# Kernel optimization log

Hardware: AMD Instinct MI355X
Metric: run time of the kernel (lower is better)

The kernel has to match this reference:

```python
import jax, jax.numpy as jnp
import numpy as np

N_QUBITS = 6
N_LAYERS = 3
FEATURE_DIM = 512
ENC_HIDDEN = max(32, N_QUBITS * 4)  # 32
HEAD_HIDDEN = 128
G, T = 54, 24
DIM = 2 ** N_QUBITS  # 64


def _ry_batched(angles):
    # angles: [B] -> batched RY matrices [B, 2, 2] (complex64)
    c = jnp.cos(angles * 0.5)
    s = jnp.sin(angles * 0.5)
    U = jnp.stack([jnp.stack([c, -s], -1), jnp.stack([s, c], -1)], -2)
    return U.astype(jnp.complex64)


def _rot(phi, theta, omega):
    # PennyLane Rot = RZ(omega) RY(theta) RZ(phi); returns [2, 2] complex64
    c = jnp.cos(theta * 0.5).astype(jnp.complex64)
    s = jnp.sin(theta * 0.5).astype(jnp.complex64)
    ep = jnp.exp(-0.5j * (phi + omega).astype(jnp.complex64))  # e^{-i(phi+omega)/2}
    em = jnp.exp(-0.5j * (phi - omega).astype(jnp.complex64))  # e^{-i(phi-omega)/2}
    u00 = ep * c
    u01 = -jnp.conj(em) * s
    u10 = em * s
    u11 = jnp.conj(ep) * c
    return jnp.stack([jnp.stack([u00, u01]), jnp.stack([u10, u11])])


def _apply_1q_batched(state, U, q):
    # state: [B, 2^n]; U: [B, 2, 2] (per-sample gate, e.g. data-encoding RY)
    B = state.shape[0]
    st = state.reshape(B, 2 ** q, 2, -1)
    st = jnp.einsum('bij,bljr->blir', U, st)
    return st.reshape(B, -1)


def _apply_1q(state, U, q):
    # state: [B, 2^n]; U: [2, 2] shared across batch (trainable Rot)
    B = state.shape[0]
    st = state.reshape(B, 2 ** q, 2, -1)
    st = jnp.einsum('ij,bljr->blir', U, st)
    return st.reshape(B, -1)


def _apply_cnot(state, c, t):
    # state: [B, 2^n]; flip target axis where control bit == 1
    B = state.shape[0]
    st = state.reshape((B,) + (2,) * N_QUBITS)
    ax_c, ax_t = 1 + c, 1 + t
    s0 = jnp.take(st, 0, axis=ax_c)
    s1 = jnp.take(st, 1, axis=ax_c)
    s1 = jnp.flip(s1, axis=ax_t if ax_t < ax_c else ax_t - 1)
    st = jnp.stack([s0, s1], axis=ax_c)
    return st.reshape(B, -1)


def _expvals_z(state):
    # <Z_q> for every qubit: [B, n]
    B = state.shape[0]
    probs = (state.real ** 2 + state.imag ** 2).reshape((B,) + (2,) * N_QUBITS)
    outs = []
    for q in range(N_QUBITS):
        axes = tuple(i for i in range(1, N_QUBITS + 1) if i != q + 1)
        p = probs.sum(axes)  # [B, 2]
        outs.append(p[:, 0] - p[:, 1])
    return jnp.stack(outs, -1)


def _circuit(angles, q_weights):
    # angles: [B, n_qubits] float32; q_weights: [L, n, 3]
    B = angles.shape[0]
    state = jnp.zeros((B, DIM), jnp.complex64).at[:, 0].set(1.0)
    for layer in range(N_LAYERS):
        # data_reuploading=True -> re-encode every layer
        for q in range(N_QUBITS):
            state = _apply_1q_batched(state, _ry_batched(angles[:, q]), q)
        for q in range(N_QUBITS):
            w = q_weights[layer, q]
            state = _apply_1q(state, _rot(w[0], w[1], w[2]), q)
        for q in range(0, N_QUBITS - 1, 2):
            state = _apply_cnot(state, q, q + 1)
        for q in range(1, N_QUBITS - 1, 2):
            state = _apply_cnot(state, q, q + 1)
        state = _apply_cnot(state, N_QUBITS - 1, 0)  # n_qubits > 2
    return _expvals_z(state)


def setup_inputs() -> dict:
    key = jax.random.key(0)
    ks = jax.random.split(key, 10)
    B = 32768
    return {
        'x': jax.random.normal(ks[0], (B, FEATURE_DIM), jnp.float32),
        'enc_w1': 0.05 * jax.random.normal(ks[1], (FEATURE_DIM, ENC_HIDDEN), jnp.float32),
        'enc_b1': jnp.zeros((ENC_HIDDEN,), jnp.float32),
        'enc_w2': 0.05 * jax.random.normal(ks[2], (ENC_HIDDEN, N_QUBITS), jnp.float32),
        'enc_b2': jnp.zeros((N_QUBITS,), jnp.float32),
        'q_weights': 0.01 * jax.random.normal(ks[3], (N_LAYERS, N_QUBITS, 3), jnp.float32),
        'head_w1': 0.1 * jax.random.normal(ks[4], (N_QUBITS, HEAD_HIDDEN), jnp.float32),
        'head_b1': jnp.zeros((HEAD_HIDDEN,), jnp.float32),
        'head_w2': 0.05 * jax.random.normal(ks[5], (HEAD_HIDDEN, G * T), jnp.float32),
        'head_b2': jnp.zeros((G * T,), jnp.float32),
    }


def reference(x, enc_w1, enc_b1, enc_w2, enc_b2, q_weights,
              head_w1, head_b1, head_w2, head_b2):
    # classical encoder -> angles [B, n_qubits]
    h = jnp.tanh(x @ enc_w1 + enc_b1)
    angles = h @ enc_w2 + enc_b2
    # batched state-vector PQC simulation
    z = _circuit(angles, q_weights).astype(jnp.float32)  # [B, n_qubits]
    # classical head (dropout is identity in eval)
    g = jax.nn.relu(z @ head_w1 + head_b1)
    logits = g @ head_w2 + head_b2
    return logits.reshape(-1, G, T)
```

## Files before the change

kernel.cpp:

```cpp
#include <hip/hip_runtime.h>

typedef __bf16 bf16x8 __attribute__((ext_vector_type(8)));
typedef float floatx4 __attribute__((ext_vector_type(4)));
typedef unsigned short ushort8 __attribute__((ext_vector_type(8)));

__device__ __forceinline__ unsigned short f2bf(float f) {
    unsigned u = __float_as_uint(f);
    u += 0x7fffu + ((u >> 16) & 1u);
    return (unsigned short)(u >> 16);
}

template <int ST>
__device__ __forceinline__ void apply_g(float* sr, float* si,
    float m00r, float m00i, float m01r, float m01i,
    float m10r, float m10i, float m11r, float m11i) {
#pragma unroll
    for (int i = 0; i < 64; ++i) {
        if ((i & ST) == 0) {
            int i1 = i + ST;
            float r0 = sr[i], u0 = si[i], r1 = sr[i1], u1 = si[i1];
            sr[i]  = m00r * r0 - m00i * u0 + m01r * r1 - m01i * u1;
            si[i]  = m00r * u0 + m00i * r0 + m01r * u1 + m01i * r1;
            sr[i1] = m10r * r0 - m10i * u0 + m11r * r1 - m11i * u1;
            si[i1] = m10r * u0 + m10i * r0 + m11r * u1 + m11i * r1;
        }
    }
}

template <int CB, int TB>
__device__ __forceinline__ void cnot_g(float* sr, float* si) {
#pragma unroll
    for (int i = 0; i < 64; ++i) {
        if ((i & CB) && !(i & TB)) {
            int i1 = i + TB;
            float tr = sr[i]; sr[i] = sr[i1]; sr[i1] = tr;
            float ti = si[i]; si[i] = si[i1]; si[i1] = ti;
        }
    }
}

__global__ __launch_bounds__(256) void fused_front(
    const float* __restrict__ x, const float* __restrict__ w1,
    const float* __restrict__ b1, const float* __restrict__ w2,
    const float* __restrict__ b2, const float* __restrict__ qw,
    const float* __restrict__ hw1, const float* __restrict__ hb1,
    const float* __restrict__ hw2,
    unsigned short* __restrict__ w2t, unsigned short* __restrict__ g) {

    if (blockIdx.x >= 512) {
        int t = (blockIdx.x - 512) * 256 + threadIdx.x;
        int nn = t >> 4;
        int kc = (t & 15) * 8;
        if (nn < 1296) {
            ushort8 pk;
#pragma unroll
            for (int j = 0; j < 8; ++j) pk[j] = f2bf(hw2[(size_t)(kc + j) * 1296 + nn]);
            *(ushort8*)(w2t + (size_t)nn * 128 + kc) = pk;
        }
        return;
    }

    __shared__ float part[4][64][33];
    __shared__ float hsh[64][33];
    __shared__ float umat_s[144];

    if (threadIdx.x < 18) {
        int t = threadIdx.x;
        float phi = qw[t * 3], theta = qw[t * 3 + 1], omega = qw[t * 3 + 2];
        float c = cosf(0.5f * theta), s = sinf(0.5f * theta);
        float po = 0.5f * (phi + omega), pm = 0.5f * (phi - omega);
        float epr = cosf(po), epi = -sinf(po);
        float emr = cosf(pm), emi = -sinf(pm);
        float* u = umat_s + t * 8;
        u[0] = epr * c;  u[1] = epi * c;
        u[2] = -emr * s; u[3] = emi * s;
        u[4] = emr * s;  u[5] = emi * s;
        u[6] = epr * c;  u[7] = -epi * c;
    }

    int lane = threadIdx.x & 63;
    int wave = threadIdx.x >> 6;
    int swave = __builtin_amdgcn_readfirstlane(wave);
    size_t row = (size_t)blockIdx.x * 64 + lane;
    const float2* x2 = (const float2*)(x + row * 512 + swave * 128);
    const float* wseg = w1 + swave * 128 * 32;

    float acc[32];
#pragma unroll
    for (int j = 0; j < 32; ++j) acc[j] = 0.f;

#pragma clang loop unroll(disable)
    for (int k2 = 0; k2 < 64; ++k2) {
        float2 xv = x2[k2];
        const float* wr = wseg + k2 * 64;
#pragma unroll
        for (int j = 0; j < 32; ++j) acc[j] = fmaf(wr[j], xv.x, acc[j]);
#pragma unroll
        for (int j = 0; j < 32; ++j) acc[j] = fmaf(wr[32 + j], xv.y, acc[j]);
    }
#pragma unroll
    for (int j = 0; j < 32; ++j) part[wave][lane][j] = acc[j];
    __syncthreads();

    int rl = threadIdx.x & 63;
    int jg = (threadIdx.x >> 6) * 8;
#pragma unroll
    for (int jj = 0; jj < 8; ++jj) {
        int j = jg + jj;
        float v = part[0][rl][j] + part[1][rl][j] + part[2][rl][j] + part[3][rl][j] + b1[j];
        hsh[rl][j] = tanhf(v);
    }
    __syncthreads();

    if (threadIdx.x >= 64) return;

    float h[32];
#pragma unroll
    for (int j = 0; j < 32; ++j) h[j] = hsh[threadIdx.x][j];
    float ca[6], sa[6];
#pragma unroll
    for (int q = 0; q < 6; ++q) {
        float a = b2[q];
#pragma unroll
        for (int j = 0; j < 32; ++j) a = fmaf(h[j], w2[j * 6 + q], a);
        a = 0.5f * a;
        ca[q] = cosf(a);
        sa[q] = sinf(a);
    }

    float sr[64], si[64];
#pragma unroll
    for (int i = 0; i < 64; ++i) { sr[i] = 0.f; si[i] = 0.f; }
    sr[0] = 1.f;

#pragma clang loop unroll(disable)
    for (int layer = 0; layer < 3; ++layer) {
        const float* ub = umat_s + layer * 48;
#define DOQ(Q, ST) {                                                      \
        const float* u = ub + (Q) * 8;                                    \
        float c = ca[Q], ss = sa[Q];                                      \
        float m00r = u[0] * c + u[2] * ss, m00i = u[1] * c + u[3] * ss;   \
        float m01r = u[2] * c - u[0] * ss, m01i = u[3] * c - u[1] * ss;   \
        float m10r = u[4] * c + u[6] * ss, m10i = u[5] * c + u[7] * ss;   \
        float m11r = u[6] * c - u[4] * ss, m11i = u[7] * c - u[5] * ss;   \
        apply_g<ST>(sr, si, m00r, m00i, m01r, m01i, m10r, m10i, m11r, m11i); }
        DOQ(0, 32) DOQ(1, 16) DOQ(2, 8) DOQ(3, 4) DOQ(4, 2) DOQ(5, 1)
#undef DOQ
        cnot_g<32, 16>(sr, si);
        cnot_g<8, 4>(sr, si);
        cnot_g<2, 1>(sr, si);
        cnot_g<16, 8>(sr, si);
        cnot_g<4, 2>(sr, si);
        cnot_g<1, 32>(sr, si);
    }

    float z[6] = {0.f, 0.f, 0.f, 0.f, 0.f, 0.f};
#pragma unroll
    for (int i = 0; i < 64; ++i) {
        float p = sr[i] * sr[i] + si[i] * si[i];
        z[0] += (i & 32) ? -p : p;
        z[1] += (i & 16) ? -p : p;
        z[2] += (i & 8)  ? -p : p;
        z[3] += (i & 4)  ? -p : p;
        z[4] += (i & 2)  ? -p : p;
        z[5] += (i & 1)  ? -p : p;
    }

    int s = blockIdx.x * 64 + threadIdx.x;
    unsigned short* gp = g + (size_t)s * 128;
#pragma unroll 2
    for (int j0 = 0; j0 < 128; j0 += 8) {
        ushort8 pk;
#pragma unroll
        for (int jj = 0; jj < 8; ++jj) {
            int j = j0 + jj;
            float a = hb1[j];
#pragma unroll
            for (int q = 0; q < 6; ++q) a = fmaf(z[q], hw1[q * 128 + j], a);
            a = fmaxf(a, 0.f);
            pk[jj] = f2bf(a);
        }
        *(ushort8*)(gp + j0) = pk;
    }
}

__global__ __launch_bounds__(256) void head_gemm(
    const unsigned short* __restrict__ g, const unsigned short* __restrict__ w2t,
    const float* __restrict__ b2, float* __restrict__ out) {
    int lane = threadIdx.x & 63;
    int task = blockIdx.x * 4 + (threadIdx.x >> 6);
    int m = task / 27;
    int n = task - m * 27;
    int row0 = m * 64, col0 = n * 48;
    int l15 = lane & 15, quad = lane >> 4;

    const unsigned short* ap = w2t + (size_t)(col0 + l15) * 128 + quad * 8;
    const unsigned short* bp = g + (size_t)(row0 + l15) * 128 + quad * 8;

    floatx4 acc[12];
#pragma unroll
    for (int i = 0; i < 12; ++i) acc[i] = (floatx4)0.f;

#pragma unroll
    for (int ks = 0; ks < 4; ++ks) {
        bf16x8 af[3], bf[4];
#pragma unroll
        for (int t = 0; t < 3; ++t) af[t] = *(const bf16x8*)(ap + (size_t)t * 16 * 128 + ks * 32);
#pragma unroll
        for (int sub = 0; sub < 4; ++sub) bf[sub] = *(const bf16x8*)(bp + (size_t)sub * 16 * 128 + ks * 32);
#pragma unroll
        for (int t = 0; t < 3; ++t)
#pragma unroll
            for (int sub = 0; sub < 4; ++sub)
                acc[t * 4 + sub] = __builtin_amdgcn_mfma_f32_16x16x32_bf16(af[t], bf[sub], acc[t * 4 + sub], 0, 0, 0);
    }

#pragma unroll
    for (int t = 0; t < 3; ++t) {
        const float* bb = b2 + col0 + t * 16 + quad * 4;
        floatx4 bias = { bb[0], bb[1], bb[2], bb[3] };
#pragma unroll
        for (int sub = 0; sub < 4; ++sub) {
            floatx4 v = acc[t * 4 + sub] + bias;
            floatx4* dst = (floatx4*)(out + (size_t)(row0 + sub * 16 + l15) * 1296 + col0 + t * 16 + quad * 4);
            __builtin_nontemporal_store(v, dst);
        }
    }
}

extern "C" void kernel_launch(void* const* d_in, const int* in_sizes, int n_in,
                              void* d_out, int out_size, void* d_ws, size_t ws_size,
                              hipStream_t stream) {
    const float* x   = (const float*)d_in[0];
    const float* ew1 = (const float*)d_in[1];
    const float* eb1 = (const float*)d_in[2];
    const float* ew2 = (const float*)d_in[3];
    const float* eb2 = (const float*)d_in[4];
    const float* qw  = (const float*)d_in[5];
    const float* hw1 = (const float*)d_in[6];
    const float* hb1 = (const float*)d_in[7];
    const float* hw2 = (const float*)d_in[8];
    const float* hb2 = (const float*)d_in[9];
    float* out = (float*)d_out;

    char* ws = (char*)d_ws;
    unsigned short* g   = (unsigned short*)(ws);
    unsigned short* w2t = (unsigned short*)(ws + 8388608);

    fused_front<<<dim3(593), dim3(256), 0, stream>>>(x, ew1, eb1, ew2, eb2, qw, hw1, hb1, hw2, w2t, g);
    head_gemm<<<dim3(3456), dim3(256), 0, stream>>>(g, w2t, hb2, out);
}
```

Before: 350.9 us.

## Split each sample's state vector across four lanes using cross-lane shuffles

The quantum circuit simulation used to run on only 64 of 256 threads, each holding a 64-amplitude state in registers. Now all 256 threads take part: each sample's state is spread over 4 lanes holding 16 amplitudes each. Gates on the top two qubits and the matching CNOTs use __shfl_xor exchanges. The angle/cos/sin computation and the head-hidden output are also split across waves. This cuts register pressure and the serial per-thread work, at the cost of shuffle traffic, an extra barrier, and more complex qubit-index bookkeeping.

```diff
diff --git a/kernel.cpp b/kernel.cpp
--- a/kernel.cpp
+++ b/kernel.cpp
@@ -11,33 +11,42 @@
 }
 
 template <int ST>
-__device__ __forceinline__ void apply_g(float* sr, float* si,
+__device__ __forceinline__ void apply_local(float* fr, float* fi,
     float m00r, float m00i, float m01r, float m01i,
     float m10r, float m10i, float m11r, float m11i) {
 #pragma unroll
-    for (int i = 0; i < 64; ++i) {
+    for (int i = 0; i < 16; ++i) {
         if ((i & ST) == 0) {
             int i1 = i + ST;
-            float r0 = sr[i], u0 = si[i], r1 = sr[i1], u1 = si[i1];
-            sr[i]  = m00r * r0 - m00i * u0 + m01r * r1 - m01i * u1;
-            si[i]  = m00r * u0 + m00i * r0 + m01r * u1 + m01i * r1;
-            sr[i1] = m10r * r0 - m10i * u0 + m11r * r1 - m11i * u1;
-            si[i1] = m10r * u0 + m10i * r0 + m11r * u1 + m11i * r1;
-        }
-    }
-}
-
-template <int CB, int TB>
-__device__ __forceinline__ void cnot_g(float* sr, float* si) {
-#pragma unroll
-    for (int i = 0; i < 64; ++i) {
-        if ((i & CB) && !(i & TB)) {
-            int i1 = i + TB;
-            float tr = sr[i]; sr[i] = sr[i1]; sr[i1] = tr;
-            float ti = si[i]; si[i] = si[i1]; si[i1] = ti;
-        }
-    }
-}
+            float r0 = fr[i], u0 = fi[i], r1 = fr[i1], u1 = fi[i1];
+            fr[i]  = m00r * r0 - m00i * u0 + m01r * r1 - m01i * u1;
+            fi[i]  = m00r * u0 + m00i * r0 + m01r * u1 + m01i * r1;
+            fr[i1] = m10r * r0 - m10i * u0 + m11r * r1 - m11i * u1;
+            fi[i1] = m10r * u0 + m10i * r0 + m11r * u1 + m11i * r1;
+        }
+    }
+}
+
+template <int XM>
+__device__ __forceinline__ void apply_cross(float* fr, float* fi, bool hi,
+    float m00r, float m00i, float m01r, float m01i,
+    float m10r, float m10i, float m11r, float m11i) {
+    float car = hi ? m10r : m00r, cai = hi ? m10i : m00i;
+    float cbr = hi ? m11r : m01r, cbi = hi ? m11i : m01i;
+#pragma unroll
+    for (int j = 0; j < 16; ++j) {
+        float mr = fr[j], mi = fi[j];
+        float pr = __shfl_xor(mr, XM);
+        float pi = __shfl_xor(mi, XM);
+        float a0r = hi ? pr : mr, a0i = hi ? pi : mi;
+        float a1r = hi ? mr : pr, a1i = hi ? mi : pi;
+        fr[j] = car * a0r - cai * a0i + cbr * a1r - cbi * a1i;
+        fi[j] = car * a0i + cai * a0r + cbr * a1i + cbi * a1r;
+    }
+}
+
+#define SWAP2(a, b) { float _t = fr[a]; fr[a] = fr[b]; fr[b] = _t; \
+                      _t = fi[a]; fi[a] = fi[b]; fi[b] = _t; }
 
 __global__ __launch_bounds__(256) void fused_front(
     const float* __restrict__ x, const float* __restrict__ w1,
@@ -63,6 +72,7 @@
     __shared__ float part[4][64][33];
     __shared__ float hsh[64][33];
     __shared__ float umat_s[144];
+    __shared__ float casa[64][12];
 
     if (threadIdx.x < 18) {
         int t = threadIdx.x;
@@ -102,81 +112,120 @@
     for (int j = 0; j < 32; ++j) part[wave][lane][j] = acc[j];
     __syncthreads();
 
-    int rl = threadIdx.x & 63;
-    int jg = (threadIdx.x >> 6) * 8;
-#pragma unroll
-    for (int jj = 0; jj < 8; ++jj) {
-        int j = jg + jj;
-        float v = part[0][rl][j] + part[1][rl][j] + part[2][rl][j] + part[3][rl][j] + b1[j];
-        hsh[rl][j] = tanhf(v);
+    {
+        int rl = threadIdx.x & 63;
+        int jg = (threadIdx.x >> 6) * 8;
+#pragma unroll
+        for (int jj = 0; jj < 8; ++jj) {
+            int j = jg + jj;
+            float v = part[0][rl][j] + part[1][rl][j] + part[2][rl][j] + part[3][rl][j] + b1[j];
+            hsh[rl][j] = tanhf(v);
+        }
     }
     __syncthreads();
 
-    if (threadIdx.x >= 64) return;
-
-    float h[32];
-#pragma unroll
-    for (int j = 0; j < 32; ++j) h[j] = hsh[threadIdx.x][j];
+    {
+        int row_a = threadIdx.x & 63;
+        for (int qq = threadIdx.x >> 6; qq < 6; qq += 4) {
+            float a = b2[qq];
+#pragma unroll
+            for (int j = 0; j < 32; ++j) a = fmaf(hsh[row_a][j], w2[j * 6 + qq], a);
+            a *= 0.5f;
+            casa[row_a][qq]     = cosf(a);
+            casa[row_a][qq + 6] = sinf(a);
+        }
+    }
+    __syncthreads();
+
+    int samp = wave * 16 + (lane & 15);
+    int p = lane >> 4;
+    bool podd = (p & 1) != 0;
+    bool phi1 = (p >> 1) != 0;
+
     float ca[6], sa[6];
 #pragma unroll
-    for (int q = 0; q < 6; ++q) {
-        float a = b2[q];
-#pragma unroll
-        for (int j = 0; j < 32; ++j) a = fmaf(h[j], w2[j * 6 + q], a);
-        a = 0.5f * a;
-        ca[q] = cosf(a);
-        sa[q] = sinf(a);
-    }
-
-    float sr[64], si[64];
-#pragma unroll
-    for (int i = 0; i < 64; ++i) { sr[i] = 0.f; si[i] = 0.f; }
-    sr[0] = 1.f;
+    for (int q = 0; q < 6; ++q) { ca[q] = casa[samp][q]; sa[q] = casa[samp][q + 6]; }
+
+    float fr[16], fi[16];
+#pragma unroll
+    for (int j = 0; j < 16; ++j) { fr[j] = 0.f; fi[j] = 0.f; }
+    fr[0] = (p == 0) ? 1.f : 0.f;
 
 #pragma clang loop unroll(disable)
     for (int layer = 0; layer < 3; ++layer) {
         const float* ub = umat_s + layer * 48;
-#define DOQ(Q, ST) {                                                      \
+#define MAT(Q)                                                            \
         const float* u = ub + (Q) * 8;                                    \
         float c = ca[Q], ss = sa[Q];                                      \
         float m00r = u[0] * c + u[2] * ss, m00i = u[1] * c + u[3] * ss;   \
         float m01r = u[2] * c - u[0] * ss, m01i = u[3] * c - u[1] * ss;   \
         float m10r = u[4] * c + u[6] * ss, m10i = u[5] * c + u[7] * ss;   \
-        float m11r = u[6] * c - u[4] * ss, m11i = u[7] * c - u[5] * ss;   \
-        apply_g<ST>(sr, si, m00r, m00i, m01r, m01i, m10r, m10i, m11r, m11i); }
-        DOQ(0, 32) DOQ(1, 16) DOQ(2, 8) DOQ(3, 4) DOQ(4, 2) DOQ(5, 1)
-#undef DOQ
-        cnot_g<32, 16>(sr, si);
-        cnot_g<8, 4>(sr, si);
-        cnot_g<2, 1>(sr, si);
-        cnot_g<16, 8>(sr, si);
-        cnot_g<4, 2>(sr, si);
-        cnot_g<1, 32>(sr, si);
-    }
-
-    float z[6] = {0.f, 0.f, 0.f, 0.f, 0.f, 0.f};
-#pragma unroll
-    for (int i = 0; i < 64; ++i) {
-        float p = sr[i] * sr[i] + si[i] * si[i];
-        z[0] += (i & 32) ? -p : p;
-        z[1] += (i & 16) ? -p : p;
-        z[2] += (i & 8)  ? -p : p;
-        z[3] += (i & 4)  ? -p : p;
-        z[4] += (i & 2)  ? -p : p;
-        z[5] += (i & 1)  ? -p : p;
-    }
-
-    int s = blockIdx.x * 64 + threadIdx.x;
-    unsigned short* gp = g + (size_t)s * 128;
-#pragma unroll 2
-    for (int j0 = 0; j0 < 128; j0 += 8) {
+        float m11r = u[6] * c - u[4] * ss, m11i = u[7] * c - u[5] * ss;
+        { MAT(0) apply_cross<32>(fr, fi, phi1, m00r, m00i, m01r, m01i, m10r, m10i, m11r, m11i); }
+        { MAT(1) apply_cross<16>(fr, fi, podd, m00r, m00i, m01r, m01i, m10r, m10i, m11r, m11i); }
+        { MAT(2) apply_local<8>(fr, fi, m00r, m00i, m01r, m01i, m10r, m10i, m11r, m11i); }
+        { MAT(3) apply_local<4>(fr, fi, m00r, m00i, m01r, m01i, m10r, m10i, m11r, m11i); }
+        { MAT(4) apply_local<2>(fr, fi, m00r, m00i, m01r, m01i, m10r, m10i, m11r, m11i); }
+        { MAT(5) apply_local<1>(fr, fi, m00r, m00i, m01r, m01i, m10r, m10i, m11r, m11i); }
+#undef MAT
+#pragma unroll
+        for (int j = 0; j < 16; ++j) {
+            float pr = __shfl_xor(fr[j], 16);
+            float pi = __shfl_xor(fi[j], 16);
+            fr[j] = phi1 ? pr : fr[j];
+            fi[j] = phi1 ? pi : fi[j];
+        }
+        SWAP2(8, 12) SWAP2(9, 13) SWAP2(10, 14) SWAP2(11, 15)
+        SWAP2(2, 3) SWAP2(6, 7) SWAP2(10, 11) SWAP2(14, 15)
+        {
+            float tr[16], ti[16];
+#pragma unroll
+            for (int j = 0; j < 16; ++j) { tr[j] = fr[j]; ti[j] = fi[j]; }
+#pragma unroll
+            for (int j = 0; j < 16; ++j) {
+                fr[j] = podd ? tr[j ^ 8] : tr[j];
+                fi[j] = podd ? ti[j ^ 8] : ti[j];
+            }
+        }
+        SWAP2(4, 6) SWAP2(5, 7) SWAP2(12, 14) SWAP2(13, 15)
+#pragma unroll
+        for (int j = 1; j < 16; j += 2) {
+            fr[j] = __shfl_xor(fr[j], 32);
+            fi[j] = __shfl_xor(fi[j], 32);
+        }
+    }
+
+    float zt = 0.f, z2 = 0.f, z3 = 0.f, z4 = 0.f, z5 = 0.f;
+#pragma unroll
+    for (int j = 0; j < 16; ++j) {
+        float pp = fr[j] * fr[j] + fi[j] * fi[j];
+        zt += pp;
+        z2 += (j & 8) ? -pp : pp;
+        z3 += (j & 4) ? -pp : pp;
+        z4 += (j & 2) ? -pp : pp;
+        z5 += (j & 1) ? -pp : pp;
+    }
+    float zz[6];
+    zz[0] = phi1 ? -zt : zt;
+    zz[1] = podd ? -zt : zt;
+    zz[2] = z2; zz[3] = z3; zz[4] = z4; zz[5] = z5;
+#pragma unroll
+    for (int q = 0; q < 6; ++q) {
+        zz[q] += __shfl_xor(zz[q], 16);
+        zz[q] += __shfl_xor(zz[q], 32);
+    }
+
+    int s = blockIdx.x * 64 + samp;
+    unsigned short* gp = g + (size_t)s * 128 + p * 32;
+#pragma unroll
+    for (int j0 = 0; j0 < 32; j0 += 8) {
         ushort8 pk;
 #pragma unroll
         for (int jj = 0; jj < 8; ++jj) {
-            int j = j0 + jj;
+            int j = p * 32 + j0 + jj;
             float a = hb1[j];
 #pragma unroll
-            for (int q = 0; q < 6; ++q) a = fmaf(z[q], hw1[q * 128 + j], a);
+            for (int q = 0; q < 6; ++q) a = fmaf(zz[q], hw1[q * 128 + j], a);
             a = fmaxf(a, 0.f);
             pk[jj] = f2bf(a);
         }
```

New measurement: 342.9 us. 2.3% less time.
